# Optimization experiments

Hardware: AMD Instinct MI355X
Metric: run time of the kernel (lower is better)

The kernel has to match this reference:

```python
import jax, jax.numpy as jnp
import numpy as np

WINDOW = (8, 8)
NUM_HEADS = 12


def setup_inputs() -> dict:
    key = jax.random.key(0)
    k0, k1, k2 = jax.random.split(key, 3)
    B_, H, W, C = 8, 64, 64, 768
    x = jax.random.normal(k0, (B_, H * W, C), dtype=jnp.float32)
    qkv_w = jax.random.normal(k1, (3 * C, C), dtype=jnp.float32) * 0.02
    qkv_b = jnp.zeros((3 * C,), dtype=jnp.float32)
    proj_w = jax.random.normal(k2, (C, C), dtype=jnp.float32) * 0.02
    proj_b = jnp.zeros((C,), dtype=jnp.float32)
    return {"x": x, "qkv_w": qkv_w, "qkv_b": qkv_b,
            "proj_w": proj_w, "proj_b": proj_b, "H": H, "W": W}


def reference(x, qkv_w, qkv_b, proj_w, proj_b, H, W):
    ws0, ws1 = WINDOW
    nh = NUM_HEADS
    B_, N, C = x.shape
    hd = C // nh
    scale = hd ** (-0.5)

    x = x.reshape(B_, H, W, C)
    # pad bottom/right so H, W divisible by window size (static Python ints)
    pad_b = (ws0 - H % ws0) % ws0
    pad_r = (ws1 - W % ws1) % ws1
    x = jnp.pad(x, ((0, 0), (0, pad_b), (0, pad_r), (0, 0)))
    Hp, Wp = H + pad_b, W + pad_r

    # window partition: (B, Hp, Wp, C) -> (B*nW, ws0*ws1, C)
    xw = (x.reshape(B_, Hp // ws0, ws0, Wp // ws1, ws1, C)
            .transpose(0, 1, 3, 2, 4, 5)
            .reshape(-1, ws0 * ws1, C))
    Bw, Nw = xw.shape[0], xw.shape[1]

    # fused qkv projection
    qkv = xw @ qkv_w.T + qkv_b                       # (Bw, Nw, 3C)
    qkv = qkv.reshape(Bw, Nw, 3, nh, hd).transpose(2, 0, 3, 1, 4)
    q, k, v = qkv[0], qkv[1], qkv[2]                 # (Bw, nh, Nw, hd)

    attn = jax.nn.softmax((q * scale) @ jnp.swapaxes(k, -2, -1), axis=-1)
    out = (attn @ v).transpose(0, 2, 1, 3).reshape(Bw, Nw, C)
    out = out @ proj_w.T + proj_b

    # window reverse: (B*nW, ws0*ws1, C) -> (B, Hp, Wp, C)
    out = (out.reshape(B_, Hp // ws0, Wp // ws1, ws0, ws1, C)
              .transpose(0, 1, 3, 2, 4, 5)
              .reshape(B_, Hp, Wp, C))
    out = out[:, :H, :W, :]
    return out.reshape(B_, H * W, C)
```

## Files before the change

### kernel.cpp

```cpp
#include <hip/hip_runtime.h>
#include <stdint.h>

typedef __attribute__((ext_vector_type(8))) __bf16 bf16x8;
typedef __attribute__((ext_vector_type(4))) float f32x4;
typedef __attribute__((ext_vector_type(8))) unsigned short u16x8;

__device__ __forceinline__ unsigned short f2bf(float f) {
  union { float f; unsigned u; } v; v.f = f;
  return (unsigned short)((v.u + 0x7FFFu + ((v.u >> 16) & 1u)) >> 16);
}

__device__ __forceinline__ void gload16(const void* g, void* l) {
  __builtin_amdgcn_global_load_lds(
      (const __attribute__((address_space(1))) void*)g,
      (__attribute__((address_space(3))) void*)l, 16, 0, 0);
}

__global__ __launch_bounds__(256) void pack_x_kernel(const float* __restrict__ x,
                                                     unsigned short* __restrict__ xw) {
  int idx = blockIdx.x * 256 + threadIdx.x;
  int m = idx / 96;
  int p = idx - m * 96;
  int win = m >> 6, tok = m & 63;
  int b = win >> 6, wh = (win >> 3) & 7, ww = win & 7;
  int r = tok >> 3, c = tok & 7;
  size_t xoff = ((size_t)b * 4096 + (wh * 8 + r) * 64 + (ww * 8 + c)) * 768 + p * 8;
  const float* src = x + xoff;
  u16x8 o;
#pragma unroll
  for (int j = 0; j < 8; ++j) o[j] = f2bf(src[j]);
  *(u16x8*)(xw + (size_t)m * 768 + p * 8) = o;
}

__global__ __launch_bounds__(256) void pack_w_kernel(const float* __restrict__ qkvw,
                                                     const float* __restrict__ projw,
                                                     unsigned short* __restrict__ wq,
                                                     unsigned short* __restrict__ wp) {
  int idx = blockIdx.x * 256 + threadIdx.x;
  const float* src;
  unsigned short* dst;
  if (idx < 221184) { src = qkvw + (size_t)idx * 8; dst = wq + (size_t)idx * 8; }
  else { int i2 = idx - 221184; src = projw + (size_t)i2 * 8; dst = wp + (size_t)i2 * 8; }
  u16x8 o;
#pragma unroll
  for (int j = 0; j < 8; ++j) o[j] = f2bf(src[j]);
  *(u16x8*)dst = o;
}

template <int N, bool PROJ>
__global__ __launch_bounds__(512) void gemm256_kernel(
    const unsigned short* __restrict__ A, const unsigned short* __restrict__ Bm,
    const float* __restrict__ bias, void* __restrict__ Cout) {
  constexpr int K = 768;
  constexpr int NT = K / 32;
  constexpr int NBN = N / 256;
  extern __shared__ char smem[];

  const int tid = threadIdx.x;
  const int wave = tid >> 6;
  const int lane = tid & 63;
  const int wm = wave >> 2;
  const int wn = wave & 3;

  const int cpx = gridDim.x >> 3;
  const int bid = (blockIdx.x & 7) * cpx + (blockIdx.x >> 3);
  const int tm = (bid / NBN) * 256;
  const int tn = (bid % NBN) * 256;

  const int c0 = tid, c1 = 512 + tid;
  const int r0 = c0 >> 2, r1 = c1 >> 2;
  const int g0 = ((c0 & 3) ^ ((c0 >> 3) & 3)) * 8;
  const int g1 = ((c1 & 3) ^ ((c1 >> 3) & 3)) * 8;
  const unsigned short* gA0 = A + (size_t)(tm + r0) * K + g0;
  const unsigned short* gA1 = A + (size_t)(tm + r1) * K + g1;
  const unsigned short* gB0 = Bm + (size_t)(tn + r0) * K + g0;
  const unsigned short* gB1 = Bm + (size_t)(tn + r1) * K + g1;
  const int ldsA0 = wave * 1024;
  const int ldsA1 = 8192 + wave * 1024;
  const int ldsB0 = 16384 + wave * 1024;
  const int ldsB1 = 24576 + wave * 1024;

  {
    char* s0 = smem;
    char* s1 = smem + 32768;
    gload16(gA0, s0 + ldsA0); gload16(gA1, s0 + ldsA1);
    gload16(gB0, s0 + ldsB0); gload16(gB1, s0 + ldsB1);
    gload16(gA0 + 32, s1 + ldsA0); gload16(gA1 + 32, s1 + ldsA1);
    gload16(gB0 + 32, s1 + ldsB0); gload16(gB1 + 32, s1 + ldsB1);
  }
  asm volatile("s_waitcnt vmcnt(4)" ::: "memory");
  asm volatile("s_barrier" ::: "memory");

  const int lrow = lane & 15;
  const int lg8 = ((lane >> 4) ^ ((lane >> 1) & 3)) * 8;

  f32x4 acc[8][4] = {};

  for (int t = 0; t < NT; ++t) {
    const unsigned short* sAt = (const unsigned short*)(smem + ((t & 3) << 15));
    const unsigned short* sBt = sAt + 8192;

    if (t + 2 < NT) {
      char* sb = smem + (((t + 2) & 3) << 15);
      gload16(gA0 + (t + 2) * 32, sb + ldsA0);
      gload16(gA1 + (t + 2) * 32, sb + ldsA1);
      gload16(gB0 + (t + 2) * 32, sb + ldsB0);
      gload16(gB1 + (t + 2) * 32, sb + ldsB1);
    }

    bf16x8 a0[4], b0[4], a1[4];
#pragma unroll
    for (int mi = 0; mi < 4; ++mi)
      a0[mi] = *(const bf16x8*)(sAt + (wm * 128 + mi * 16 + lrow) * 32 + lg8);
#pragma unroll
    for (int ni = 0; ni < 4; ++ni)
      b0[ni] = *(const bf16x8*)(sBt + (wn * 64 + ni * 16 + lrow) * 32 + lg8);
#pragma unroll
    for (int mi = 0; mi < 4; ++mi)
      a1[mi] = *(const bf16x8*)(sAt + (wm * 128 + 64 + mi * 16 + lrow) * 32 + lg8);

    if (t < NT - 2)
      asm volatile("s_waitcnt vmcnt(4)" ::: "memory");
    else if (t == NT - 2)
      asm volatile("s_waitcnt vmcnt(0)" ::: "memory");
    asm volatile("s_barrier" ::: "memory");

    __builtin_amdgcn_s_setprio(1);
#pragma unroll
    for (int mi = 0; mi < 4; ++mi)
#pragma unroll
      for (int ni = 0; ni < 4; ++ni)
        acc[mi][ni] = __builtin_amdgcn_mfma_f32_16x16x32_bf16(a0[mi], b0[ni], acc[mi][ni], 0, 0, 0);
#pragma unroll
    for (int mi = 0; mi < 4; ++mi)
#pragma unroll
      for (int ni = 0; ni < 4; ++ni)
        acc[4 + mi][ni] = __builtin_amdgcn_mfma_f32_16x16x32_bf16(a1[mi], b0[ni], acc[4 + mi][ni], 0, 0, 0);
    __builtin_amdgcn_s_setprio(0);
  }

  const int crow = tm + wm * 128 + ((lane >> 4) << 2);
  const int ccol0 = tn + wn * 64 + lrow;
  if constexpr (!PROJ) {
    unsigned short* C = (unsigned short*)Cout;
#pragma unroll
    for (int ni = 0; ni < 4; ++ni) {
      const int col = ccol0 + ni * 16;
      const float bv = bias[col];
#pragma unroll
      for (int mi = 0; mi < 8; ++mi)
#pragma unroll
        for (int r = 0; r < 4; ++r)
          C[(size_t)(crow + mi * 16 + r) * N + col] = f2bf(acc[mi][ni][r] + bv);
    }
  } else {
    float* out = (float*)Cout;
#pragma unroll
    for (int mi = 0; mi < 8; ++mi)
#pragma unroll
      for (int r = 0; r < 4; ++r) {
        int m = crow + mi * 16 + r;
        int win = m >> 6, tok = m & 63;
        int bb = win >> 6, wh = (win >> 3) & 7, ww = win & 7;
        int rr = tok >> 3, cc = tok & 7;
        float* op = out + ((size_t)bb * 4096 + (wh * 8 + rr) * 64 + (ww * 8 + cc)) * 768;
#pragma unroll
        for (int ni = 0; ni < 4; ++ni) {
          int col = ccol0 + ni * 16;
          op[col] = acc[mi][ni][r] + bias[col];
        }
      }
  }
}

__global__ __launch_bounds__(64) void attn_kernel(const unsigned short* __restrict__ qkv,
                                                  unsigned short* __restrict__ attnout) {
  __shared__ unsigned short sQ[64 * 64];
  __shared__ unsigned short sK[64 * 64];
  __shared__ unsigned short sVT[64 * 64];
  const int lane = threadIdx.x;
  const int win = blockIdx.x / 12;
  const int head = blockIdx.x - win * 12;
  const size_t row0 = (size_t)win * 64;
  const int qoff = head * 64, koff = 768 + head * 64, voff = 1536 + head * 64;

#pragma unroll
  for (int i = 0; i < 8; ++i) {
    int e = lane + i * 64;
    int row = e >> 3, cb = (e & 7) * 8;
    gload16(qkv + (row0 + row) * 2304 + qoff + cb, (char*)sQ + i * 1024);
    gload16(qkv + (row0 + row) * 2304 + koff + cb, (char*)sK + i * 1024);
  }
  {
    const unsigned short* gv = qkv + (row0 + lane) * 2304 + voff;
#pragma unroll
    for (int j = 0; j < 8; ++j) {
      u16x8 v = *(const u16x8*)(gv + j * 8);
#pragma unroll
      for (int d = 0; d < 8; ++d) sVT[(j * 8 + d) * 64 + lane] = v[d];
    }
  }
  __syncthreads();

  const int lrow = lane & 15;
  const int lkb = (lane >> 4) * 8;

  f32x4 s[4][4] = {};
#pragma unroll
  for (int ks = 0; ks < 2; ++ks) {
    bf16x8 qf[4], kf[4];
#pragma unroll
    for (int mi = 0; mi < 4; ++mi) qf[mi] = *(const bf16x8*)&sQ[(mi * 16 + lrow) * 64 + ks * 32 + lkb];
#pragma unroll
    for (int ni = 0; ni < 4; ++ni) kf[ni] = *(const bf16x8*)&sK[(ni * 16 + lrow) * 64 + ks * 32 + lkb];
#pragma unroll
    for (int mi = 0; mi < 4; ++mi)
#pragma unroll
      for (int ni = 0; ni < 4; ++ni)
        s[mi][ni] = __builtin_amdgcn_mfma_f32_16x16x32_bf16(qf[mi], kf[ni], s[mi][ni], 0, 0, 0);
  }

  float p[4][4][4];
#pragma unroll
  for (int mi = 0; mi < 4; ++mi) {
#pragma unroll
    for (int r = 0; r < 4; ++r) {
      float v0 = s[mi][0][r] * 0.125f, v1 = s[mi][1][r] * 0.125f;
      float v2 = s[mi][2][r] * 0.125f, v3 = s[mi][3][r] * 0.125f;
      float mx = fmaxf(fmaxf(v0, v1), fmaxf(v2, v3));
      mx = fmaxf(mx, __shfl_xor(mx, 1));
      mx = fmaxf(mx, __shfl_xor(mx, 2));
      mx = fmaxf(mx, __shfl_xor(mx, 4));
      mx = fmaxf(mx, __shfl_xor(mx, 8));
      float e0 = __expf(v0 - mx), e1 = __expf(v1 - mx);
      float e2 = __expf(v2 - mx), e3 = __expf(v3 - mx);
      float sm = e0 + e1 + e2 + e3;
      sm += __shfl_xor(sm, 1);
      sm += __shfl_xor(sm, 2);
      sm += __shfl_xor(sm, 4);
      sm += __shfl_xor(sm, 8);
      float inv = 1.0f / sm;
      p[mi][0][r] = e0 * inv; p[mi][1][r] = e1 * inv;
      p[mi][2][r] = e2 * inv; p[mi][3][r] = e3 * inv;
    }
  }

  __syncthreads();
#pragma unroll
  for (int mi = 0; mi < 4; ++mi)
#pragma unroll
    for (int ni = 0; ni < 4; ++ni)
#pragma unroll
      for (int r = 0; r < 4; ++r)
        sK[(mi * 16 + (lane >> 4) * 4 + r) * 64 + ni * 16 + lrow] = f2bf(p[mi][ni][r]);
  __syncthreads();

  f32x4 o[4][4] = {};
#pragma unroll
  for (int ks = 0; ks < 2; ++ks) {
    bf16x8 pf[4], vf[4];
#pragma unroll
    for (int mi = 0; mi < 4; ++mi) pf[mi] = *(const bf16x8*)&sK[(mi * 16 + lrow) * 64 + ks * 32 + lkb];
#pragma unroll
    for (int ni = 0; ni < 4; ++ni) vf[ni] = *(const bf16x8*)&sVT[(ni * 16 + lrow) * 64 + ks * 32 + lkb];
#pragma unroll
    for (int mi = 0; mi < 4; ++mi)
#pragma unroll
      for (int ni = 0; ni < 4; ++ni)
        o[mi][ni] = __builtin_amdgcn_mfma_f32_16x16x32_bf16(pf[mi], vf[ni], o[mi][ni], 0, 0, 0);
  }

#pragma unroll
  for (int mi = 0; mi < 4; ++mi)
#pragma unroll
    for (int ni = 0; ni < 4; ++ni) {
      int col = head * 64 + ni * 16 + lrow;
#pragma unroll
      for (int r = 0; r < 4; ++r) {
        int trow = mi * 16 + (lane >> 4) * 4 + r;
        attnout[(row0 + trow) * 768 + col] = f2bf(o[mi][ni][r]);
      }
    }
}

extern "C" void kernel_launch(void* const* d_in, const int* in_sizes, int n_in,
                              void* d_out, int out_size, void* d_ws, size_t ws_size,
                              hipStream_t stream) {
  (void)in_sizes; (void)n_in; (void)out_size; (void)ws_size;
  const float* x = (const float*)d_in[0];
  const float* qkv_w = (const float*)d_in[1];
  const float* qkv_b = (const float*)d_in[2];
  const float* proj_w = (const float*)d_in[3];
  const float* proj_b = (const float*)d_in[4];
  float* out = (float*)d_out;

  char* ws = (char*)d_ws;
  unsigned short* xw   = (unsigned short*)(ws);
  unsigned short* qkvB = (unsigned short*)(ws + 50331648);
  unsigned short* wq   = (unsigned short*)(ws + 50331648 + 150994944);
  unsigned short* wp   = (unsigned short*)(ws + 50331648 + 150994944 + 3538944);

  (void)hipFuncSetAttribute((const void*)(gemm256_kernel<2304, false>),
                            hipFuncAttributeMaxDynamicSharedMemorySize, 131072);
  (void)hipFuncSetAttribute((const void*)(gemm256_kernel<768, true>),
                            hipFuncAttributeMaxDynamicSharedMemorySize, 131072);

  pack_x_kernel<<<12288, 256, 0, stream>>>(x, xw);
  pack_w_kernel<<<1152, 256, 0, stream>>>(qkv_w, proj_w, wq, wp);
  gemm256_kernel<2304, false><<<1152, 512, 131072, stream>>>(xw, wq, qkv_b, qkvB);
  attn_kernel<<<6144, 64, 0, stream>>>(qkvB, xw);
  gemm256_kernel<768, true><<<384, 512, 131072, stream>>>(xw, wp, proj_b, out);
}
```

Baseline: 282.6 us.

## Software-pipeline LDS fragment loads and vectorize transposed GEMM epilogue stores

Restructures the GEMM main loop so that the next tile's A0/B fragments are prefetched from LDS after the barrier, while the current tile's MFMAs run. The global-to-LDS loads for A and B are split around the first MFMA batch. The MFMA operands are swapped so each lane holds 4 consecutive columns, which lets the epilogue write packed bf16x4 and float4 stores instead of scalar ones. It also adds a launch_bounds occupancy hint and fully unrolls the K loop, which raises register pressure and code size.

Result: no change. 282.7 us (+0.1%).

```diff
diff --git a/kernel.cpp b/kernel.cpp
--- a/kernel.cpp
+++ b/kernel.cpp
@@ -4,6 +4,7 @@
 typedef __attribute__((ext_vector_type(8))) __bf16 bf16x8;
 typedef __attribute__((ext_vector_type(4))) float f32x4;
 typedef __attribute__((ext_vector_type(8))) unsigned short u16x8;
+typedef __attribute__((ext_vector_type(2))) unsigned int u32x2;
 
 __device__ __forceinline__ unsigned short f2bf(float f) {
   union { float f; unsigned u; } v; v.f = f;
@@ -48,7 +49,7 @@
 }
 
 template <int N, bool PROJ>
-__global__ __launch_bounds__(512) void gemm256_kernel(
+__global__ __launch_bounds__(512, 2) void gemm256_kernel(
     const unsigned short* __restrict__ A, const unsigned short* __restrict__ Bm,
     const float* __restrict__ bias, void* __restrict__ Cout) {
   constexpr int K = 768;
@@ -80,6 +81,9 @@
   const int ldsB0 = 16384 + wave * 1024;
   const int ldsB1 = 24576 + wave * 1024;
 
+  const int lrow = lane & 15;
+  const int lg8 = ((lane >> 4) ^ ((lane >> 1) & 3)) * 8;
+
   {
     char* s0 = smem;
     char* s1 = smem + 32768;
@@ -91,85 +95,111 @@
   asm volatile("s_waitcnt vmcnt(4)" ::: "memory");
   asm volatile("s_barrier" ::: "memory");
 
-  const int lrow = lane & 15;
-  const int lg8 = ((lane >> 4) ^ ((lane >> 1) & 3)) * 8;
-
   f32x4 acc[8][4] = {};
 
+  bf16x8 a0[4], b[4];
+  {
+    const unsigned short* s0 = (const unsigned short*)smem;
+#pragma unroll
+    for (int mi = 0; mi < 4; ++mi)
+      a0[mi] = *(const bf16x8*)(s0 + (wm * 128 + mi * 16 + lrow) * 32 + lg8);
+#pragma unroll
+    for (int ni = 0; ni < 4; ++ni)
+      b[ni] = *(const bf16x8*)(s0 + 8192 + (wn * 64 + ni * 16 + lrow) * 32 + lg8);
+  }
+
+#pragma unroll
   for (int t = 0; t < NT; ++t) {
     const unsigned short* sAt = (const unsigned short*)(smem + ((t & 3) << 15));
-    const unsigned short* sBt = sAt + 8192;
 
     if (t + 2 < NT) {
       char* sb = smem + (((t + 2) & 3) << 15);
       gload16(gA0 + (t + 2) * 32, sb + ldsA0);
       gload16(gA1 + (t + 2) * 32, sb + ldsA1);
+    }
+    bf16x8 a1[4];
+#pragma unroll
+    for (int mi = 0; mi < 4; ++mi)
+      a1[mi] = *(const bf16x8*)(sAt + (wm * 128 + 64 + mi * 16 + lrow) * 32 + lg8);
+
+    __builtin_amdgcn_s_setprio(1);
+#pragma unroll
+    for (int mi = 0; mi < 4; ++mi)
+#pragma unroll
+      for (int ni = 0; ni < 4; ++ni)
+        acc[mi][ni] = __builtin_amdgcn_mfma_f32_16x16x32_bf16(b[ni], a0[mi], acc[mi][ni], 0, 0, 0);
+    __builtin_amdgcn_s_setprio(0);
+
+    if (t + 2 < NT) {
+      char* sb = smem + (((t + 2) & 3) << 15);
       gload16(gB0 + (t + 2) * 32, sb + ldsB0);
       gload16(gB1 + (t + 2) * 32, sb + ldsB1);
     }
-
-    bf16x8 a0[4], b0[4], a1[4];
-#pragma unroll
-    for (int mi = 0; mi < 4; ++mi)
-      a0[mi] = *(const bf16x8*)(sAt + (wm * 128 + mi * 16 + lrow) * 32 + lg8);
-#pragma unroll
-    for (int ni = 0; ni < 4; ++ni)
-      b0[ni] = *(const bf16x8*)(sBt + (wn * 64 + ni * 16 + lrow) * 32 + lg8);
-#pragma unroll
-    for (int mi = 0; mi < 4; ++mi)
-      a1[mi] = *(const bf16x8*)(sAt + (wm * 128 + 64 + mi * 16 + lrow) * 32 + lg8);
-
     if (t < NT - 2)
       asm volatile("s_waitcnt vmcnt(4)" ::: "memory");
     else if (t == NT - 2)
       asm volatile("s_waitcnt vmcnt(0)" ::: "memory");
-    asm volatile("s_barrier" ::: "memory");
+    if (t < NT - 1)
+      asm volatile("s_barrier" ::: "memory");
+
+    bf16x8 a0n[4], bn[4];
+    if (t + 1 < NT) {
+      const unsigned short* sN = (const unsigned short*)(smem + (((t + 1) & 3) << 15));
+#pragma unroll
+      for (int mi = 0; mi < 4; ++mi)
+        a0n[mi] = *(const bf16x8*)(sN + (wm * 128 + mi * 16 + lrow) * 32 + lg8);
+#pragma unroll
+      for (int ni = 0; ni < 4; ++ni)
+        bn[ni] = *(const bf16x8*)(sN + 8192 + (wn * 64 + ni * 16 + lrow) * 32 + lg8);
+    }
 
     __builtin_amdgcn_s_setprio(1);
 #pragma unroll
     for (int mi = 0; mi < 4; ++mi)
 #pragma unroll
       for (int ni = 0; ni < 4; ++ni)
-        acc[mi][ni] = __builtin_amdgcn_mfma_f32_16x16x32_bf16(a0[mi], b0[ni], acc[mi][ni], 0, 0, 0);
-#pragma unroll
-    for (int mi = 0; mi < 4; ++mi)
-#pragma unroll
-      for (int ni = 0; ni < 4; ++ni)
-        acc[4 + mi][ni] = __builtin_amdgcn_mfma_f32_16x16x32_bf16(a1[mi], b0[ni], acc[4 + mi][ni], 0, 0, 0);
+        acc[4 + mi][ni] = __builtin_amdgcn_mfma_f32_16x16x32_bf16(b[ni], a1[mi], acc[4 + mi][ni], 0, 0, 0);
     __builtin_amdgcn_s_setprio(0);
-  }
-
-  const int crow = tm + wm * 128 + ((lane >> 4) << 2);
-  const int ccol0 = tn + wn * 64 + lrow;
+
+#pragma unroll
+    for (int i = 0; i < 4; ++i) { a0[i] = a0n[i]; b[i] = bn[i]; }
+  }
+
+  const int erow = tm + wm * 128 + (lane & 15);
+  const int ecol = tn + wn * 64 + ((lane >> 4) << 2);
   if constexpr (!PROJ) {
     unsigned short* C = (unsigned short*)Cout;
 #pragma unroll
     for (int ni = 0; ni < 4; ++ni) {
-      const int col = ccol0 + ni * 16;
-      const float bv = bias[col];
-#pragma unroll
-      for (int mi = 0; mi < 8; ++mi)
-#pragma unroll
-        for (int r = 0; r < 4; ++r)
-          C[(size_t)(crow + mi * 16 + r) * N + col] = f2bf(acc[mi][ni][r] + bv);
+      const int col0 = ecol + ni * 16;
+      const f32x4 bv = *(const f32x4*)&bias[col0];
+#pragma unroll
+      for (int mi = 0; mi < 8; ++mi) {
+        f32x4 v = acc[mi][ni];
+        u32x2 pk;
+        pk.x = (unsigned)f2bf(v[0] + bv[0]) | ((unsigned)f2bf(v[1] + bv[1]) << 16);
+        pk.y = (unsigned)f2bf(v[2] + bv[2]) | ((unsigned)f2bf(v[3] + bv[3]) << 16);
+        *(u32x2*)(C + (size_t)(erow + mi * 16) * N + col0) = pk;
+      }
     }
   } else {
     float* out = (float*)Cout;
-#pragma unroll
-    for (int mi = 0; mi < 8; ++mi)
-#pragma unroll
-      for (int r = 0; r < 4; ++r) {
-        int m = crow + mi * 16 + r;
-        int win = m >> 6, tok = m & 63;
-        int bb = win >> 6, wh = (win >> 3) & 7, ww = win & 7;
-        int rr = tok >> 3, cc = tok & 7;
-        float* op = out + ((size_t)bb * 4096 + (wh * 8 + rr) * 64 + (ww * 8 + cc)) * 768;
-#pragma unroll
-        for (int ni = 0; ni < 4; ++ni) {
-          int col = ccol0 + ni * 16;
-          op[col] = acc[mi][ni][r] + bias[col];
-        }
+    f32x4 bv[4];
+#pragma unroll
+    for (int ni = 0; ni < 4; ++ni) bv[ni] = *(const f32x4*)&bias[ecol + ni * 16];
+#pragma unroll
+    for (int mi = 0; mi < 8; ++mi) {
+      int m = erow + mi * 16;
+      int win = m >> 6, tok = m & 63;
+      int bb = win >> 6, wh = (win >> 3) & 7, ww = win & 7;
+      int rr = tok >> 3, cc = tok & 7;
+      float* op = out + ((size_t)bb * 4096 + (wh * 8 + rr) * 64 + (ww * 8 + cc)) * 768;
+#pragma unroll
+      for (int ni = 0; ni < 4; ++ni) {
+        f32x4 o = acc[mi][ni] + bv[ni];
+        *(f32x4*)(op + ecol + ni * 16) = o;
       }
+    }
   }
 }
 
```
